# Kernel optimization log

Measured on AMD Instinct MI355X. Metric: run time of the kernel, lower is better.

Reference implementation:

```python
import jax, jax.numpy as jnp
import numpy as np

N, E, IN, H, C, ED = 50000, 800000, 128, 4, 64, 4
NEG_SLOPE = 0.2


def setup_inputs() -> dict:
    key = jax.random.key(0)
    ks = iter(jax.random.split(key, 40))
    def p(shape, s=0.05):
        return jax.random.normal(next(ks), shape, jnp.float32) * s
    inp = dict(
        x=jax.random.normal(next(ks), (N, IN), jnp.float32),
        edge_index=jax.random.randint(next(ks), (2, E), 0, N),
        edge_attr=jax.random.normal(next(ks), (E, ED), jnp.float32),
        # GATConv layer 1 (concat=True)
        W1=p((IN, H * C)), att_src1=p((H, C)), att_dst1=p((H, C)),
        We1=p((ED, H * C)), att_e1=p((H, C)), b1=p((H * C,)),
        g1=jnp.ones((H * C,), jnp.float32), be1=jnp.zeros((H * C,), jnp.float32),
        # GATConv layer 2 (concat=False -> mean over heads)
        W2=p((H * C, H * C)), att_src2=p((H, C)), att_dst2=p((H, C)),
        We2=p((ED, H * C)), att_e2=p((H, C)), b2=p((C,)),
        g2=jnp.ones((C,), jnp.float32), be2=jnp.zeros((C,), jnp.float32),
        # skip / MLP head
        skip_W=p((IN, C)), skip_b=p((C,)),
        fc1_W=p((C, C // 2)), fc1_b=p((C // 2,)),
        fc2_W=p((C // 2, 1)), fc2_b=p((1,)),
    )
    return inp


def _add_self_loops(edge_index, edge_attr, n):
    # PyG GATConv default: add_self_loops=True, fill_value='mean'
    src, dst = edge_index[0], edge_index[1]
    sums = jax.ops.segment_sum(edge_attr, dst, num_segments=n)
    cnt = jax.ops.segment_sum(jnp.ones((edge_attr.shape[0], 1), edge_attr.dtype), dst, num_segments=n)
    mean_attr = sums / jnp.maximum(cnt, 1.0)
    loop = jnp.arange(n)
    src = jnp.concatenate([src, loop])
    dst = jnp.concatenate([dst, loop])
    ea = jnp.concatenate([edge_attr, mean_attr], axis=0)
    return src, dst, ea


def _gat_layer(x, src, dst, ea, W, a_src, a_dst, We, a_e, bias, n, concat):
    xs = (x @ W).reshape(n, H, C)                     # [N,H,C]
    alpha_src = (xs * a_src).sum(-1)                  # [N,H]
    alpha_dst = (xs * a_dst).sum(-1)                  # [N,H]
    ep = (ea @ We).reshape(-1, H, C)                  # [Et,H,C]
    alpha_e = (ep * a_e).sum(-1)                      # [Et,H]
    alpha = jax.nn.leaky_relu(alpha_src[src] + alpha_dst[dst] + alpha_e, NEG_SLOPE)
    # segment softmax over destination nodes
    m = jax.ops.segment_max(alpha, dst, num_segments=n)
    alpha = jnp.exp(alpha - m[dst])
    denom = jax.ops.segment_sum(alpha, dst, num_segments=n)
    alpha = alpha / (denom[dst] + 1e-16)
    out = jax.ops.segment_sum(xs[src] * alpha[:, :, None], dst, num_segments=n)  # [N,H,C]
    out = out.reshape(n, H * C) if concat else out.mean(axis=1)
    return out + bias


def _bn(x, g, b):
    mu = x.mean(0)
    var = x.var(0)
    return (x - mu) * jax.lax.rsqrt(var + 1e-5) * g + b


def reference(x, edge_index, edge_attr, W1, att_src1, att_dst1, We1, att_e1, b1, g1, be1,
              W2, att_src2, att_dst2, We2, att_e2, b2, g2, be2,
              skip_W, skip_b, fc1_W, fc1_b, fc2_W, fc2_b):
    n = x.shape[0]
    src, dst, ea = _add_self_loops(edge_index, edge_attr, n)
    residual = x @ skip_W + skip_b
    h = _gat_layer(x, src, dst, ea, W1, att_src1, att_dst1, We1, att_e1, b1, n, True)
    h = jax.nn.elu(_bn(h, g1, be1))
    h = _gat_layer(h, src, dst, ea, W2, att_src2, att_dst2, We2, att_e2, b2, n, False)
    h = jax.nn.elu(_bn(h, g2, be2))
    h = h + residual
    h = jax.nn.relu(h @ fc1_W + fc1_b)
    h = jax.nn.softplus(h @ fc2_W + fc2_b)
    return h.squeeze(-1)
```

## Files before the change

kernel.cpp:

```cpp
#include <hip/hip_runtime.h>
#include <math.h>

static constexpr int N_NODES = 50000;
static constexpr int N_EDGES = 800000;
static constexpr int IN_F = 128;
static constexpr int CH = 64;
static constexpr int HC = 256;
static constexpr float NEG_SLOPE = 0.2f;

typedef __attribute__((ext_vector_type(8))) short bf16x8;
typedef __attribute__((ext_vector_type(4))) float f32x4;

__device__ __forceinline__ unsigned pack_bf(float a, float b) {
    unsigned ua = __float_as_uint(a) + 0x8000u;
    unsigned ub = __float_as_uint(b) + 0x8000u;
    return __builtin_amdgcn_perm(ub, ua, 0x07060302u);
}
__device__ __forceinline__ float bflo(unsigned u) { return __uint_as_float(u << 16); }
__device__ __forceinline__ float bfhi(unsigned u) { return __uint_as_float(u & 0xffff0000u); }
__device__ __forceinline__ float bfs(unsigned short u) {
    return __uint_as_float((unsigned)u << 16);
}
__device__ __forceinline__ float elu(float v) { return v > 0.f ? v : expm1f(v); }

__global__ void csr_hist(const int* __restrict__ ei, int* __restrict__ deg) {
    int e = blockIdx.x * blockDim.x + threadIdx.x;
    if (e >= N_EDGES) return;
    atomicAdd(&deg[ei[N_EDGES + e]], 1);
}

__global__ void scan_block(const int* __restrict__ deg, int* __restrict__ rowptr,
                           int* __restrict__ bsum) {
    __shared__ int s[256];
    int tid = threadIdx.x;
    int i = blockIdx.x * 256 + tid;
    int v = (i < N_NODES) ? deg[i] : 0;
    s[tid] = v;
    __syncthreads();
    for (int off = 1; off < 256; off <<= 1) {
        int t = (tid >= off) ? s[tid - off] : 0;
        __syncthreads();
        s[tid] += t;
        __syncthreads();
    }
    if (i < N_NODES) rowptr[i] = s[tid] - v;
    if (tid == 255) bsum[blockIdx.x] = s[255];
}

__global__ void scan_bsum(int* __restrict__ bsum, int nb) {
    __shared__ int s[256];
    int tid = threadIdx.x;
    int v = (tid < nb) ? bsum[tid] : 0;
    s[tid] = v;
    __syncthreads();
    for (int off = 1; off < 256; off <<= 1) {
        int t = (tid >= off) ? s[tid - off] : 0;
        __syncthreads();
        s[tid] += t;
        __syncthreads();
    }
    if (tid < nb) bsum[tid] = s[tid] - v;
}

__global__ void scan_add(int* __restrict__ rowptr, const int* __restrict__ bsum,
                         int* __restrict__ fillc) {
    int i = blockIdx.x * blockDim.x + threadIdx.x;
    if (i < N_NODES) {
        rowptr[i] += bsum[i >> 8];
        fillc[i] = 0;
    }
    if (i == N_NODES) rowptr[N_NODES] = N_EDGES;
}

__global__ void csr_fill(const int* __restrict__ ei, const int* __restrict__ rowptr,
                         int* __restrict__ fillc, int* __restrict__ csr_src,
                         int* __restrict__ pos) {
    int e = blockIdx.x * blockDim.x + threadIdx.x;
    if (e >= N_EDGES) return;
    int s = ei[e];
    int t = ei[N_EDGES + e];
    int p = atomicAdd(&fillc[t], 1);
    int i = rowptr[t] + p;
    csr_src[i] = s;
    pos[e] = i;
}

__global__ void conv_all(const float* __restrict__ W1, const float* __restrict__ W2,
                         const float* __restrict__ Ws, const float* __restrict__ We1,
                         const float* __restrict__ atte1, const float* __restrict__ We2,
                         const float* __restrict__ atte2, unsigned short* __restrict__ WT1,
                         unsigned short* __restrict__ WT2, unsigned short* __restrict__ WTs,
                         float* __restrict__ weff) {
    int t = blockIdx.x * blockDim.x + threadIdx.x;
    if (t < 32768) {
        int k = t >> 8, n = t & 255;
        unsigned u = __float_as_uint(W1[t]) + 0x8000u;
        WT1[n * 128 + k] = (unsigned short)(u >> 16);
    } else if (t < 98304) {
        int u2 = t - 32768;
        int k = u2 >> 8, n = u2 & 255;
        unsigned u = __float_as_uint(W2[u2]) + 0x8000u;
        WT2[n * 256 + k] = (unsigned short)(u >> 16);
    } else if (t < 106496) {
        int u2 = t - 98304;
        int k = u2 >> 6, n = u2 & 63;
        unsigned u = __float_as_uint(Ws[u2]) + 0x8000u;
        WTs[n * 128 + k] = (unsigned short)(u >> 16);
    } else if (t < 106496 + 32) {
        int idx = t - 106496;
        const float* We = idx < 16 ? We1 : We2;
        const float* ae = idx < 16 ? atte1 : atte2;
        int j = idx & 15;
        int d = j >> 2, h = j & 3;
        float s = 0.f;
        for (int c = 0; c < CH; ++c) s += We[d * HC + h * CH + c] * ae[h * CH + c];
        weff[idx] = s;
    }
}

template <int K, bool ABF, bool BN>
__global__ __launch_bounds__(256) void gemm_mfma_att(
    const void* __restrict__ Av, const unsigned short* __restrict__ BT,
    const float* __restrict__ scale, const float* __restrict__ shift,
    const float* __restrict__ att_src, const float* __restrict__ att_dst,
    unsigned short* __restrict__ xsb, float* __restrict__ asrc, float* __restrict__ adst,
    int M) {
    constexpr int RT = 2, NT = 16;
    const int lane = threadIdx.x & 63;
    const int wid = threadIdx.x >> 6;
    const int r0 = blockIdx.x * (4 * RT * 16) + wid * RT * 16;
    const int lr = lane & 15;
    const int kg = lane >> 4;
    f32x4 acc[RT][NT] = {};
    const float* af = (const float*)Av;
    const unsigned short* ab = (const unsigned short*)Av;
    size_t rowoff[RT];
#pragma unroll
    for (int m = 0; m < RT; ++m) {
        int r = r0 + m * 16 + lr;
        if (r >= M) r = M - 1;
        rowoff[m] = (size_t)r * K + kg * 8;
    }
    const unsigned short* brow = BT + (size_t)lr * K + kg * 8;
    for (int k0 = 0; k0 < K; k0 += 32) {
        float4 sc0, sc1, sh0, sh1;
        if constexpr (BN) {
            sc0 = *reinterpret_cast<const float4*>(scale + k0 + kg * 8);
            sc1 = *reinterpret_cast<const float4*>(scale + k0 + kg * 8 + 4);
            sh0 = *reinterpret_cast<const float4*>(shift + k0 + kg * 8);
            sh1 = *reinterpret_cast<const float4*>(shift + k0 + kg * 8 + 4);
        }
        bf16x8 a[RT];
#pragma unroll
        for (int m = 0; m < RT; ++m) {
            if constexpr (!ABF) {
                const float4 lo = *reinterpret_cast<const float4*>(af + rowoff[m] + k0);
                const float4 hi = *reinterpret_cast<const float4*>(af + rowoff[m] + k0 + 4);
                union { bf16x8 v; unsigned u[4]; } fa;
                fa.u[0] = pack_bf(lo.x, lo.y);
                fa.u[1] = pack_bf(lo.z, lo.w);
                fa.u[2] = pack_bf(hi.x, hi.y);
                fa.u[3] = pack_bf(hi.z, hi.w);
                a[m] = fa.v;
            } else {
                union { bf16x8 v; unsigned short us[8]; unsigned u[4]; } fa;
                fa.v = *reinterpret_cast<const bf16x8*>(ab + rowoff[m] + k0);
                if constexpr (BN) {
                    float f0 = elu(fmaf(bfs(fa.us[0]), sc0.x, sh0.x));
                    float f1 = elu(fmaf(bfs(fa.us[1]), sc0.y, sh0.y));
                    float f2 = elu(fmaf(bfs(fa.us[2]), sc0.z, sh0.z));
                    float f3 = elu(fmaf(bfs(fa.us[3]), sc0.w, sh0.w));
                    float f4 = elu(fmaf(bfs(fa.us[4]), sc1.x, sh1.x));
                    float f5 = elu(fmaf(bfs(fa.us[5]), sc1.y, sh1.y));
                    float f6 = elu(fmaf(bfs(fa.us[6]), sc1.z, sh1.z));
                    float f7 = elu(fmaf(bfs(fa.us[7]), sc1.w, sh1.w));
                    fa.u[0] = pack_bf(f0, f1);
                    fa.u[1] = pack_bf(f2, f3);
                    fa.u[2] = pack_bf(f4, f5);
                    fa.u[3] = pack_bf(f6, f7);
                }
                a[m] = fa.v;
            }
        }
#pragma unroll
        for (int c = 0; c < NT; ++c) {
            bf16x8 b = *reinterpret_cast<const bf16x8*>(brow + (size_t)c * 16 * K + k0);
#pragma unroll
            for (int m = 0; m < RT; ++m)
                acc[m][c] = __builtin_amdgcn_mfma_f32_16x16x32_bf16(a[m], b, acc[m][c], 0, 0, 0);
        }
    }
    float attS[NT], attD[NT];
#pragma unroll
    for (int c = 0; c < NT; ++c) {
        attS[c] = att_src[c * 16 + lr];
        attD[c] = att_dst[c * 16 + lr];
    }
#pragma unroll
    for (int m = 0; m < RT; ++m) {
        int rbase = r0 + m * 16 + kg * 4;
#pragma unroll
        for (int j = 0; j < 4; ++j) {
            int row = rbase + j;
            bool valid = row < M;
#pragma unroll
            for (int c = 0; c < NT; ++c) {
                unsigned u = __float_as_uint(acc[m][c][j]) + 0x8000u;
                if (valid) xsb[(size_t)row * HC + c * 16 + lr] = (unsigned short)(u >> 16);
            }
#pragma unroll
            for (int h = 0; h < 4; ++h) {
                float ps = acc[m][4 * h + 0][j] * attS[4 * h + 0] +
                           acc[m][4 * h + 1][j] * attS[4 * h + 1] +
                           acc[m][4 * h + 2][j] * attS[4 * h + 2] +
                           acc[m][4 * h + 3][j] * attS[4 * h + 3];
                float pd = acc[m][4 * h + 0][j] * attD[4 * h + 0] +
                           acc[m][4 * h + 1][j] * attD[4 * h + 1] +
                           acc[m][4 * h + 2][j] * attD[4 * h + 2] +
                           acc[m][4 * h + 3][j] * attD[4 * h + 3];
#pragma unroll
                for (int mk = 1; mk < 16; mk <<= 1) {
                    ps += __shfl_xor(ps, mk);
                    pd += __shfl_xor(pd, mk);
                }
                if (valid && lr == 0) {
                    asrc[row * 4 + h] = ps;
                    adst[row * 4 + h] = pd;
                }
            }
        }
    }
}

template <int K, int NT, int RT>
__global__ __launch_bounds__(256) void gemm_mfma_bias(const float* __restrict__ A,
                                                      const unsigned short* __restrict__ BT,
                                                      const float* __restrict__ bias,
                                                      float* __restrict__ C, int M) {
    const int lane = threadIdx.x & 63;
    const int wid = threadIdx.x >> 6;
    const int r0 = blockIdx.x * (4 * RT * 16) + wid * RT * 16;
    const int lr = lane & 15;
    const int kg = lane >> 4;
    f32x4 acc[RT][NT] = {};
    const float* arow[RT];
#pragma unroll
    for (int m = 0; m < RT; ++m) {
        int r = r0 + m * 16 + lr;
        if (r >= M) r = M - 1;
        arow[m] = A + (size_t)r * K + kg * 8;
    }
    const unsigned short* brow = BT + (size_t)lr * K + kg * 8;
    for (int k0 = 0; k0 < K; k0 += 32) {
        bf16x8 a[RT];
#pragma unroll
        for (int m = 0; m < RT; ++m) {
            const float4 lo = *reinterpret_cast<const float4*>(arow[m] + k0);
            const float4 hi = *reinterpret_cast<const float4*>(arow[m] + k0 + 4);
            union { bf16x8 v; unsigned u[4]; } fa;
            fa.u[0] = pack_bf(lo.x, lo.y);
            fa.u[1] = pack_bf(lo.z, lo.w);
            fa.u[2] = pack_bf(hi.x, hi.y);
            fa.u[3] = pack_bf(hi.z, hi.w);
            a[m] = fa.v;
        }
#pragma unroll
        for (int c = 0; c < NT; ++c) {
            bf16x8 b = *reinterpret_cast<const bf16x8*>(brow + (size_t)c * 16 * K + k0);
#pragma unroll
            for (int m = 0; m < RT; ++m)
                acc[m][c] = __builtin_amdgcn_mfma_f32_16x16x32_bf16(a[m], b, acc[m][c], 0, 0, 0);
        }
    }
#pragma unroll
    for (int m = 0; m < RT; ++m) {
        int rbase = r0 + m * 16 + kg * 4;
#pragma unroll
        for (int c = 0; c < NT; ++c) {
            int col = c * 16 + lr;
            float bv = bias[col];
#pragma unroll
            for (int j = 0; j < 4; ++j) {
                int r = rbase + j;
                if (r < M) C[(size_t)r * (NT * 16) + col] = acc[m][c][j] + bv;
            }
        }
    }
}

__global__ __launch_bounds__(256) void edge_w(
    const int* __restrict__ ei, const float4* __restrict__ ea, const int* __restrict__ pos,
    const float* __restrict__ weff, const float4* __restrict__ asrcv,
    const float4* __restrict__ adstv, uint4* __restrict__ pw) {
    int e = blockIdx.x * blockDim.x + threadIdx.x;
    if (e >= N_EDGES) return;
    int s = ei[e];
    int t = ei[N_EDGES + e];
    const float4 v = ea[e];
    const float4 as4 = asrcv[s];
    const float4 ad4 = adstv[t];
    const float asl[4] = {as4.x, as4.y, as4.z, as4.w};
    const float adl[4] = {ad4.x, ad4.y, ad4.z, ad4.w};
    float p[4], aev[4];
#pragma unroll
    for (int h = 0; h < 4; ++h) {
        float ae = v.x * weff[h] + v.y * weff[4 + h] + v.z * weff[8 + h] + v.w * weff[12 + h];
        float l = asl[h] + adl[h] + ae;
        l = fmaxf(l, NEG_SLOPE * l);
        p[h] = __expf(l);
        aev[h] = ae;
    }
    pw[pos[e]] = make_uint4(pack_bf(p[0], p[1]), pack_bf(p[2], p[3]),
                            pack_bf(aev[0], aev[1]), pack_bf(aev[2], aev[3]));
}

template <bool MEAN>
__global__ __launch_bounds__(256) void gat_node(
    const int* __restrict__ rowptr, const int* __restrict__ csr_src,
    const uint4* __restrict__ pw, const float4* __restrict__ asrcv,
    const float4* __restrict__ adstv, const uint2* __restrict__ xsb,
    void* __restrict__ outp) {
    int t = blockIdx.x * 4 + (threadIdx.x >> 6);
    if (t >= N_NODES) return;
    const int lane = threadIdx.x & 63;
    const int h = lane >> 4;
    const unsigned sh = (h & 1) ? 0u : 16u;
    const bool hiW = (h & 2) != 0;
    const int start = rowptr[t], end = rowptr[t + 1];
    const int deg = end - start;
    float acc0 = 0.f, acc1 = 0.f, acc2 = 0.f, acc3 = 0.f;
    float psum = 0.f, aesum = 0.f;
    int i = start;
    for (; i + 8 <= end; i += 8) {
        uint2 f[8];
        float p[8], ae[8];
#pragma unroll
        for (int j = 0; j < 8; ++j) {
            int s = csr_src[i + j];
            f[j] = xsb[(size_t)s * 64 + lane];
            const uint4 w = pw[i + j];
            unsigned pword = hiW ? w.y : w.x;
            unsigned aeword = hiW ? w.w : w.z;
            p[j] = __uint_as_float((pword << sh) & 0xffff0000u);
            ae[j] = __uint_as_float((aeword << sh) & 0xffff0000u);
        }
#pragma unroll
        for (int j = 0; j < 8; ++j) {
            psum += p[j];
            aesum += ae[j];
            acc0 += bflo(f[j].x) * p[j];
            acc1 += bfhi(f[j].x) * p[j];
            acc2 += bflo(f[j].y) * p[j];
            acc3 += bfhi(f[j].y) * p[j];
        }
    }
    for (; i < end; ++i) {
        int s = csr_src[i];
        uint2 f = xsb[(size_t)s * 64 + lane];
        const uint4 w = pw[i];
        unsigned pword = hiW ? w.y : w.x;
        unsigned aeword = hiW ? w.w : w.z;
        float p = __uint_as_float((pword << sh) & 0xffff0000u);
        float ae = __uint_as_float((aeword << sh) & 0xffff0000u);
        psum += p;
        aesum += ae;
        acc0 += bflo(f.x) * p;
        acc1 += bfhi(f.x) * p;
        acc2 += bflo(f.y) * p;
        acc3 += bfhi(f.y) * p;
    }
    const float inv_deg = deg > 0 ? 1.0f / (float)deg : 1.0f;
    const float4 as4 = asrcv[t];
    const float4 ad4 = adstv[t];
    float asl = h == 0 ? as4.x : h == 1 ? as4.y : h == 2 ? as4.z : as4.w;
    float adl = h == 0 ? ad4.x : h == 1 ? ad4.y : h == 2 ? ad4.z : ad4.w;
    float l = asl + adl + aesum * inv_deg;
    l = fmaxf(l, NEG_SLOPE * l);
    const float pself = __expf(l);
    uint2 sf = xsb[(size_t)t * 64 + lane];
    acc0 += bflo(sf.x) * pself;
    acc1 += bfhi(sf.x) * pself;
    acc2 += bflo(sf.y) * pself;
    acc3 += bfhi(sf.y) * pself;
    const float inv = 1.0f / (psum + pself + 1e-16f);
    acc0 *= inv; acc1 *= inv; acc2 *= inv; acc3 *= inv;
    if constexpr (MEAN) {
        acc0 += __shfl_xor(acc0, 16); acc0 += __shfl_xor(acc0, 32);
        acc1 += __shfl_xor(acc1, 16); acc1 += __shfl_xor(acc1, 32);
        acc2 += __shfl_xor(acc2, 16); acc2 += __shfl_xor(acc2, 32);
        acc3 += __shfl_xor(acc3, 16); acc3 += __shfl_xor(acc3, 32);
        if (lane < 16) {
            float4 o = make_float4(0.25f * acc0, 0.25f * acc1, 0.25f * acc2, 0.25f * acc3);
            reinterpret_cast<float4*>(outp)[(size_t)t * 16 + lane] = o;
        }
    } else {
        reinterpret_cast<uint2*>(outp)[(size_t)t * 64 + lane] =
            make_uint2(pack_bf(acc0, acc1), pack_bf(acc2, acc3));
    }
}

__global__ void colstats_bf(const unsigned short* __restrict__ X, float* __restrict__ sum,
                            float* __restrict__ sumsq, int M) {
    int c = threadIdx.x;
    int r0 = blockIdx.x * 256;
    int r1 = min(M, r0 + 256);
    float s = 0.f, q = 0.f;
    for (int r = r0; r < r1; ++r) {
        float v = bfs(X[(size_t)r * HC + c]);
        s += v;
        q += v * v;
    }
    atomicAdd(&sum[c], s);
    atomicAdd(&sumsq[c], q);
}

template <int F>
__global__ void colstats(const float* __restrict__ X, float* __restrict__ sum,
                         float* __restrict__ sumsq, int M) {
    const int NG = 256 / F;
    int c = threadIdx.x % F;
    int g = threadIdx.x / F;
    int r0 = blockIdx.x * 256;
    int r1 = min(M, r0 + 256);
    float s = 0.f, q = 0.f;
    for (int r = r0 + g; r < r1; r += NG) {
        float v = X[(size_t)r * F + c];
        s += v;
        q += v * v;
    }
    atomicAdd(&sum[c], s);
    atomicAdd(&sumsq[c], q);
}

__global__ void bn_finalize(const float* __restrict__ sum, const float* __restrict__ sumsq,
                            const float* __restrict__ g, const float* __restrict__ be,
                            float* __restrict__ scale, float* __restrict__ shift, int F,
                            float invM) {
    int c = blockIdx.x * blockDim.x + threadIdx.x;
    if (c >= F) return;
    float mean = sum[c] * invM;
    float var = sumsq[c] * invM - mean * mean;
    float sc = g[c] * rsqrtf(var + 1e-5f);
    scale[c] = sc;
    shift[c] = be[c] - mean * sc;
}

__global__ __launch_bounds__(256) void head_mlp(
    const float* __restrict__ h2, const float* __restrict__ scale,
    const float* __restrict__ shift, const float* __restrict__ residual,
    const float* __restrict__ fc1W, const float* __restrict__ fc1b,
    const float* __restrict__ fc2W, const float* __restrict__ fc2b,
    float* __restrict__ out) {
    int n = blockIdx.x * 4 + (threadIdx.x >> 6);
    if (n >= N_NODES) return;
    int w = threadIdx.x >> 6;
    int lane = threadIdx.x & 63;
    __shared__ float hrow[4][64];
    float v = fmaf(h2[(size_t)n * CH + lane], scale[lane], shift[lane]);
    v = elu(v) + residual[(size_t)n * CH + lane];
    hrow[w][lane] = v;
    float p = 0.f;
    if (lane < 32) {
        float acc = fc1b[lane];
#pragma unroll
        for (int k = 0; k < CH; ++k) acc = fmaf(hrow[w][k], fc1W[k * 32 + lane], acc);
        acc = fmaxf(acc, 0.f);
        p = acc * fc2W[lane];
    }
    for (int off = 16; off > 0; off >>= 1) p += __shfl_down(p, off);
    if (lane == 0) {
        float z = p + fc2b[0];
        out[n] = z > 20.f ? z : log1pf(expf(z));
    }
}

extern "C" void kernel_launch(void* const* d_in, const int* in_sizes, int n_in, void* d_out,
                              int out_size, void* d_ws, size_t ws_size, hipStream_t stream) {
    const float* x        = (const float*)d_in[0];
    const int*   ei       = (const int*)d_in[1];
    const float* ea       = (const float*)d_in[2];
    const float* W1       = (const float*)d_in[3];
    const float* att_src1 = (const float*)d_in[4];
    const float* att_dst1 = (const float*)d_in[5];
    const float* We1      = (const float*)d_in[6];
    const float* att_e1   = (const float*)d_in[7];
    const float* g1       = (const float*)d_in[9];
    const float* be1      = (const float*)d_in[10];
    const float* W2       = (const float*)d_in[11];
    const float* att_src2 = (const float*)d_in[12];
    const float* att_dst2 = (const float*)d_in[13];
    const float* We2      = (const float*)d_in[14];
    const float* att_e2   = (const float*)d_in[15];
    const float* g2       = (const float*)d_in[17];
    const float* be2      = (const float*)d_in[18];
    const float* skip_W   = (const float*)d_in[19];
    const float* skip_b   = (const float*)d_in[20];
    const float* fc1_W    = (const float*)d_in[21];
    const float* fc1_b    = (const float*)d_in[22];
    const float* fc2_W    = (const float*)d_in[23];
    const float* fc2_b    = (const float*)d_in[24];
    float* out = (float*)d_out;

    float* wsf = (float*)d_ws;
    size_t off = 0;
    auto take = [&](size_t n) {
        float* p = wsf + off;
        off += n;
        return p;
    };
    unsigned short* xsb  = (unsigned short*)take((size_t)N_NODES * HC / 2);
    unsigned short* aggb = (unsigned short*)take((size_t)N_NODES * HC / 2);
    uint4* pw       = (uint4*)take((size_t)N_EDGES * 4);
    int* csr_src    = (int*)take(N_EDGES);
    int* pos        = (int*)take(N_EDGES);
    int* rowptr     = (int*)take(N_NODES + 1);
    int* degfill    = (int*)take(N_NODES);
    int* bsum       = (int*)take(256);
    float* asrc     = take(N_NODES * 4);
    float* adst     = take(N_NODES * 4);
    float* residual = take((size_t)N_NODES * CH);
    float* h2       = take((size_t)N_NODES * CH);
    float* weff     = take(32);
    float* colsum   = take(HC);
    float* colsq    = take(HC);
    float* scaleb   = take(HC);
    float* shiftb   = take(HC);
    unsigned short* WT1 = (unsigned short*)take(IN_F * HC / 2);
    unsigned short* WT2 = (unsigned short*)take(HC * HC / 2);
    unsigned short* WTs = (unsigned short*)take(IN_F * CH / 2);

    const int EB = (N_EDGES + 255) / 256;
    const int NBLK = (N_NODES + 255) / 256;
    const int NODE4 = (N_NODES + 3) / 4;

    hipMemsetAsync(degfill, 0, N_NODES * sizeof(int), stream);
    csr_hist<<<EB, 256, 0, stream>>>(ei, degfill);
    scan_block<<<NBLK, 256, 0, stream>>>(degfill, rowptr, bsum);
    scan_bsum<<<1, 256, 0, stream>>>(bsum, NBLK);
    scan_add<<<(N_NODES + 256) / 256, 256, 0, stream>>>(rowptr, bsum, degfill);
    csr_fill<<<EB, 256, 0, stream>>>(ei, rowptr, degfill, csr_src, pos);

    conv_all<<<(106528 + 255) / 256, 256, 0, stream>>>(W1, W2, skip_W, We1, att_e1, We2,
                                                       att_e2, WT1, WT2, WTs, weff);

    gemm_mfma_bias<IN_F, 4, 4><<<(N_NODES + 255) / 256, 256, 0, stream>>>(
        x, WTs, skip_b, residual, N_NODES);

    gemm_mfma_att<IN_F, false, false><<<(N_NODES + 127) / 128, 256, 0, stream>>>(
        x, WT1, nullptr, nullptr, att_src1, att_dst1, xsb, asrc, adst, N_NODES);
    edge_w<<<EB, 256, 0, stream>>>(ei, (const float4*)ea, pos, weff, (const float4*)asrc,
                                   (const float4*)adst, pw);
    gat_node<false><<<NODE4, 256, 0, stream>>>(rowptr, csr_src, pw, (const float4*)asrc,
                                               (const float4*)adst, (const uint2*)xsb, aggb);
    hipMemsetAsync(colsum, 0, 2 * HC * sizeof(float), stream);
    colstats_bf<<<NBLK, 256, 0, stream>>>(aggb, colsum, colsq, N_NODES);
    bn_finalize<<<1, HC, 0, stream>>>(colsum, colsq, g1, be1, scaleb, shiftb, HC,
                                      1.0f / N_NODES);

    gemm_mfma_att<HC, true, true><<<(N_NODES + 127) / 128, 256, 0, stream>>>(
        aggb, WT2, scaleb, shiftb, att_src2, att_dst2, xsb, asrc, adst, N_NODES);
    edge_w<<<EB, 256, 0, stream>>>(ei, (const float4*)ea, pos, weff + 16, (const float4*)asrc,
                                   (const float4*)adst, pw);
    gat_node<true><<<NODE4, 256, 0, stream>>>(rowptr, csr_src, pw, (const float4*)asrc,
                                              (const float4*)adst, (const uint2*)xsb, h2);
    hipMemsetAsync(colsum, 0, 2 * HC * sizeof(float), stream);
    colstats<CH><<<NBLK, 256, 0, stream>>>(h2, colsum, colsq, N_NODES);
    bn_finalize<<<1, CH, 0, stream>>>(colsum, colsq, g2, be2, scaleb, shiftb, CH,
                                      1.0f / N_NODES);

    head_mlp<<<NODE4, 256, 0, stream>>>(h2, scaleb, shiftb, residual, fc1_W, fc1_b,
                                        fc2_W, fc2_b, out);
}
```

Baseline: 544.8 us.

## Permute bf16 feature layout for vectorized GEMM stores and gather

Stores the projected node features in a permuted column order so each GEMM lane writes two contiguous 16-byte chunks instead of sixteen scattered 2-byte stores. The permutation is propagated through W2's transposed layout, the BN1 gamma/beta indexing and the gat_node head mapping (head becomes lane&3) and mean reduction. The scalar tail loop in gat_node is also replaced with a predicated 8-wide batch. The change couples several kernels, so any slip in the permutation bookkeeping would break correctness.

```diff
diff --git a/kernel.cpp b/kernel.cpp
--- a/kernel.cpp
+++ b/kernel.cpp
@@ -22,6 +22,8 @@
     return __uint_as_float((unsigned)u << 16);
 }
 __device__ __forceinline__ float elu(float v) { return v > 0.f ? v : expm1f(v); }
+
+__device__ __forceinline__ int sigma(int p) { return ((p & 15) << 4) | (p >> 4); }
 
 __global__ void csr_hist(const int* __restrict__ ei, int* __restrict__ deg) {
     int e = blockIdx.x * blockDim.x + threadIdx.x;
@@ -100,7 +102,7 @@
         int u2 = t - 32768;
         int k = u2 >> 8, n = u2 & 255;
         unsigned u = __float_as_uint(W2[u2]) + 0x8000u;
-        WT2[n * 256 + k] = (unsigned short)(u >> 16);
+        WT2[n * 256 + sigma(k)] = (unsigned short)(u >> 16);
     } else if (t < 106496) {
         int u2 = t - 98304;
         int k = u2 >> 6, n = u2 & 63;
@@ -198,15 +200,23 @@
     }
 #pragma unroll
     for (int m = 0; m < RT; ++m) {
-        int rbase = r0 + m * 16 + kg * 4;
 #pragma unroll
         for (int j = 0; j < 4; ++j) {
-            int row = rbase + j;
+            int row = r0 + m * 16 + kg * 4 + j;
             bool valid = row < M;
-#pragma unroll
-            for (int c = 0; c < NT; ++c) {
-                unsigned u = __float_as_uint(acc[m][c][j]) + 0x8000u;
-                if (valid) xsb[(size_t)row * HC + c * 16 + lr] = (unsigned short)(u >> 16);
+            uint4 ua, ub;
+            ua.x = pack_bf(acc[m][0][j], acc[m][1][j]);
+            ua.y = pack_bf(acc[m][2][j], acc[m][3][j]);
+            ua.z = pack_bf(acc[m][4][j], acc[m][5][j]);
+            ua.w = pack_bf(acc[m][6][j], acc[m][7][j]);
+            ub.x = pack_bf(acc[m][8][j], acc[m][9][j]);
+            ub.y = pack_bf(acc[m][10][j], acc[m][11][j]);
+            ub.z = pack_bf(acc[m][12][j], acc[m][13][j]);
+            ub.w = pack_bf(acc[m][14][j], acc[m][15][j]);
+            if (valid) {
+                uint4* dst = reinterpret_cast<uint4*>(xsb + (size_t)row * HC) + lr * 2;
+                dst[0] = ua;
+                dst[1] = ub;
             }
 #pragma unroll
             for (int h = 0; h < 4; ++h) {
@@ -323,11 +333,12 @@
     int t = blockIdx.x * 4 + (threadIdx.x >> 6);
     if (t >= N_NODES) return;
     const int lane = threadIdx.x & 63;
-    const int h = lane >> 4;
+    const int h = lane & 3;
     const unsigned sh = (h & 1) ? 0u : 16u;
     const bool hiW = (h & 2) != 0;
     const int start = rowptr[t], end = rowptr[t + 1];
     const int deg = end - start;
+    const uint2* xl = xsb + lane;
     float acc0 = 0.f, acc1 = 0.f, acc2 = 0.f, acc3 = 0.f;
     float psum = 0.f, aesum = 0.f;
     int i = start;
@@ -337,7 +348,7 @@
 #pragma unroll
         for (int j = 0; j < 8; ++j) {
             int s = csr_src[i + j];
-            f[j] = xsb[(size_t)s * 64 + lane];
+            f[j] = xl[(size_t)s * 64];
             const uint4 w = pw[i + j];
             unsigned pword = hiW ? w.y : w.x;
             unsigned aeword = hiW ? w.w : w.z;
@@ -354,20 +365,31 @@
             acc3 += bfhi(f[j].y) * p[j];
         }
     }
-    for (; i < end; ++i) {
-        int s = csr_src[i];
-        uint2 f = xsb[(size_t)s * 64 + lane];
-        const uint4 w = pw[i];
-        unsigned pword = hiW ? w.y : w.x;
-        unsigned aeword = hiW ? w.w : w.z;
-        float p = __uint_as_float((pword << sh) & 0xffff0000u);
-        float ae = __uint_as_float((aeword << sh) & 0xffff0000u);
-        psum += p;
-        aesum += ae;
-        acc0 += bflo(f.x) * p;
-        acc1 += bfhi(f.x) * p;
-        acc2 += bflo(f.y) * p;
-        acc3 += bfhi(f.y) * p;
+    if (i < end) {
+        uint2 f[8];
+        float p[8], ae[8];
+#pragma unroll
+        for (int j = 0; j < 8; ++j) {
+            int ij = i + j;
+            int idx = ij < end ? ij : end - 1;
+            int s = csr_src[idx];
+            f[j] = xl[(size_t)s * 64];
+            const uint4 w = pw[idx];
+            unsigned pword = hiW ? w.y : w.x;
+            unsigned aeword = hiW ? w.w : w.z;
+            bool valid = ij < end;
+            p[j] = valid ? __uint_as_float((pword << sh) & 0xffff0000u) : 0.f;
+            ae[j] = valid ? __uint_as_float((aeword << sh) & 0xffff0000u) : 0.f;
+        }
+#pragma unroll
+        for (int j = 0; j < 8; ++j) {
+            psum += p[j];
+            aesum += ae[j];
+            acc0 += bflo(f[j].x) * p[j];
+            acc1 += bfhi(f[j].x) * p[j];
+            acc2 += bflo(f[j].y) * p[j];
+            acc3 += bfhi(f[j].y) * p[j];
+        }
     }
     const float inv_deg = deg > 0 ? 1.0f / (float)deg : 1.0f;
     const float4 as4 = asrcv[t];
@@ -377,7 +399,7 @@
     float l = asl + adl + aesum * inv_deg;
     l = fmaxf(l, NEG_SLOPE * l);
     const float pself = __expf(l);
-    uint2 sf = xsb[(size_t)t * 64 + lane];
+    uint2 sf = xl[(size_t)t * 64];
     acc0 += bflo(sf.x) * pself;
     acc1 += bfhi(sf.x) * pself;
     acc2 += bflo(sf.y) * pself;
@@ -385,13 +407,17 @@
     const float inv = 1.0f / (psum + pself + 1e-16f);
     acc0 *= inv; acc1 *= inv; acc2 *= inv; acc3 *= inv;
     if constexpr (MEAN) {
-        acc0 += __shfl_xor(acc0, 16); acc0 += __shfl_xor(acc0, 32);
-        acc1 += __shfl_xor(acc1, 16); acc1 += __shfl_xor(acc1, 32);
-        acc2 += __shfl_xor(acc2, 16); acc2 += __shfl_xor(acc2, 32);
-        acc3 += __shfl_xor(acc3, 16); acc3 += __shfl_xor(acc3, 32);
-        if (lane < 16) {
-            float4 o = make_float4(0.25f * acc0, 0.25f * acc1, 0.25f * acc2, 0.25f * acc3);
-            reinterpret_cast<float4*>(outp)[(size_t)t * 16 + lane] = o;
+        acc0 += __shfl_xor(acc0, 1); acc0 += __shfl_xor(acc0, 2);
+        acc1 += __shfl_xor(acc1, 1); acc1 += __shfl_xor(acc1, 2);
+        acc2 += __shfl_xor(acc2, 1); acc2 += __shfl_xor(acc2, 2);
+        acc3 += __shfl_xor(acc3, 1); acc3 += __shfl_xor(acc3, 2);
+        if (h == 0) {
+            int q = lane >> 2;
+            float* o = reinterpret_cast<float*>(outp) + (size_t)t * CH + q;
+            o[0] = 0.25f * acc0;
+            o[16] = 0.25f * acc1;
+            o[32] = 0.25f * acc2;
+            o[48] = 0.25f * acc3;
         }
     } else {
         reinterpret_cast<uint2*>(outp)[(size_t)t * 64 + lane] =
@@ -432,17 +458,19 @@
     atomicAdd(&sumsq[c], q);
 }
 
+template <bool PERM>
 __global__ void bn_finalize(const float* __restrict__ sum, const float* __restrict__ sumsq,
                             const float* __restrict__ g, const float* __restrict__ be,
                             float* __restrict__ scale, float* __restrict__ shift, int F,
                             float invM) {
     int c = blockIdx.x * blockDim.x + threadIdx.x;
     if (c >= F) return;
+    int tc = PERM ? sigma(c) : c;
     float mean = sum[c] * invM;
     float var = sumsq[c] * invM - mean * mean;
-    float sc = g[c] * rsqrtf(var + 1e-5f);
+    float sc = g[tc] * rsqrtf(var + 1e-5f);
     scale[c] = sc;
-    shift[c] = be[c] - mean * sc;
+    shift[c] = be[tc] - mean * sc;
 }
 
 __global__ __launch_bounds__(256) void head_mlp(
@@ -554,8 +582,8 @@
                                                (const float4*)adst, (const uint2*)xsb, aggb);
     hipMemsetAsync(colsum, 0, 2 * HC * sizeof(float), stream);
     colstats_bf<<<NBLK, 256, 0, stream>>>(aggb, colsum, colsq, N_NODES);
-    bn_finalize<<<1, HC, 0, stream>>>(colsum, colsq, g1, be1, scaleb, shiftb, HC,
-                                      1.0f / N_NODES);
+    bn_finalize<true><<<1, HC, 0, stream>>>(colsum, colsq, g1, be1, scaleb, shiftb, HC,
+                                            1.0f / N_NODES);
 
     gemm_mfma_att<HC, true, true><<<(N_NODES + 127) / 128, 256, 0, stream>>>(
         aggb, WT2, scaleb, shiftb, att_src2, att_dst2, xsb, asrc, adst, N_NODES);
@@ -565,8 +593,8 @@
                                               (const float4*)adst, (const uint2*)xsb, h2);
     hipMemsetAsync(colsum, 0, 2 * HC * sizeof(float), stream);
     colstats<CH><<<NBLK, 256, 0, stream>>>(h2, colsum, colsq, N_NODES);
-    bn_finalize<<<1, CH, 0, stream>>>(colsum, colsq, g2, be2, scaleb, shiftb, CH,
-                                      1.0f / N_NODES);
+    bn_finalize<false><<<1, CH, 0, stream>>>(colsum, colsq, g2, be2, scaleb, shiftb, CH,
+                                             1.0f / N_NODES);
 
     head_mlp<<<NODE4, 256, 0, stream>>>(h2, scaleb, shiftb, residual, fc1_W, fc1_b,
                                         fc2_W, fc2_b, out);
```

After: 554.3 us. Within noise of the previous version (+1.7%).
